# Kernel tuning notes

Measured on AMD Instinct MI355X. Metric: run time of the kernel, lower is better.

## Reference

```python
import jax, jax.numpy as jnp
import numpy as np

E = 2  # expand_ratio


def _linear_scan(u, a):
    """h_t = a_t * h_{t-1} + u_t along axis 0, h_{-1}=0. Parallel associative scan."""
    def comb(x, y):
        a1, b1 = x
        a2, b2 = y
        return a2 * a1, a2 * b1 + b2
    _, h = jax.lax.associative_scan(comb, (a, u), axis=0)
    return h


def setup_inputs() -> dict:
    key = jax.random.key(0)
    ks = jax.random.split(key, 8)
    n, b, d = 2048, 4, 1024
    s = 1.0 / np.sqrt(d)
    return {
        "x": jax.random.normal(ks[0], (n, b, d), jnp.float32),
        "lower_bound": jax.random.uniform(ks[1], (d,), jnp.float32),
        "W_in": jax.random.normal(ks[2], (d, 3 * d), jnp.float32) * s,
        "b_in": jnp.zeros((3 * d,), jnp.float32),
        "W_out": jax.random.normal(ks[3], (d, d), jnp.float32) * s,
        "b_out": jnp.zeros((d,), jnp.float32),
        "gamma": jnp.ones((d,), jnp.float32),
        "beta": jnp.zeros((d,), jnp.float32),
    }


def reference(x, lower_bound, W_in, b_in, W_out, b_out, gamma, beta):
    n, b, d = x.shape
    h = d // E
    feat = x @ W_in + b_in                      # (n,b,3d)
    inp, og, fg = jnp.split(feat, 3, axis=-1)
    inp = jax.nn.silu(inp)
    og = jax.nn.sigmoid(og)
    fg = jax.nn.sigmoid(fg)
    # reshape (h d) -> h, d=E
    inp = inp.reshape(n, b, h, E)
    og = og.reshape(n, b, h, E)
    fg = fg.reshape(n, b, h, E)
    lb = lower_bound.reshape(h, E)
    lam = lb + (1.0 - lb) * fg                  # (n,b,h,E)
    # outer-product input: (1-lam) outer inp over the E dims -> (n,b,h,E,E)
    u = jnp.einsum('nbhd,nbhe->nbhde', 1.0 - lam, inp)
    a = jnp.broadcast_to(lam[..., None], u.shape)
    u = u.reshape(n, b, h * E * E)
    a = a.reshape(n, b, h * E * E)
    state_fwd = _linear_scan(u, a)
    state_rev = jnp.flip(_linear_scan(jnp.flip(u, 0), jnp.flip(a, 0)), 0)
    state = (state_fwd + state_rev).reshape(n, b, h, E, E)
    out = jnp.einsum('nbhde,nbhd->nbhe', state, og).reshape(n, b, d)
    # layernorm over last dim
    mu = jnp.mean(out, axis=-1, keepdims=True)
    var = jnp.var(out, axis=-1, keepdims=True)
    out = (out - mu) * jax.lax.rsqrt(var + 1e-5) * gamma + beta
    return out @ W_out + b_out
```

## Files before the change

kernel.cpp:

```cpp
#include <hip/hip_runtime.h>

typedef __bf16 bf16x8 __attribute__((ext_vector_type(8)));
typedef float floatx4 __attribute__((ext_vector_type(4)));

#define NCH 128
#define CLEN 16

__device__ __forceinline__ unsigned short f2bf(float f) {
  unsigned int u = __builtin_bit_cast(unsigned int, f);
  u += 0x7fff + ((u >> 16) & 1);
  return (unsigned short)(u >> 16);
}
__device__ __forceinline__ float bf2f(unsigned short u) {
  unsigned int v = (unsigned int)u << 16;
  return __builtin_bit_cast(float, v);
}
__device__ __forceinline__ float bf2f_lo(unsigned int u) {
  return __builtin_bit_cast(float, u << 16);
}
__device__ __forceinline__ float bf2f_hi(unsigned int u) {
  return __builtin_bit_cast(float, u & 0xffff0000u);
}

__device__ __forceinline__ void async_copy16(const void* g, void* l) {
  __builtin_amdgcn_global_load_lds(
      (const __attribute__((address_space(1))) unsigned int*)g,
      (__attribute__((address_space(3))) unsigned int*)l, 16, 0, 0);
}

__global__ void cast_x_kernel(const float* __restrict__ in, unsigned short* __restrict__ out) {
  int i = blockIdx.x * blockDim.x + threadIdx.x;
  float4 v = ((const float4*)in)[i];
  ushort4 o;
  o.x = f2bf(v.x); o.y = f2bf(v.y); o.z = f2bf(v.z); o.w = f2bf(v.w);
  ((ushort4*)out)[i] = o;
}

__global__ void tcast2_kernel(const float* __restrict__ Win, unsigned short* __restrict__ winT,
                              const float* __restrict__ Wout, unsigned short* __restrict__ woutT) {
  __shared__ float tile[32][33];
  int bx = blockIdx.x;
  const float* W;
  unsigned short* WT;
  int ncols, n0;
  if (bx < 96) { W = Win; WT = winT; ncols = 3072; n0 = bx * 32; }
  else { W = Wout; WT = woutT; ncols = 1024; n0 = (bx - 96) * 32; }
  int k0 = blockIdx.y * 32;
  int tx = threadIdx.x, ty = threadIdx.y;
  tile[ty][tx] = W[(size_t)(k0 + ty) * ncols + n0 + tx];
  __syncthreads();
  WT[(size_t)(n0 + ty) * 1024 + k0 + tx] = f2bf(tile[tx][ty]);
}

template <int EPI>
__global__ __launch_bounds__(256) void gemm_kernel(
    const unsigned short* __restrict__ A, const unsigned short* __restrict__ BT,
    const float* __restrict__ bias, const float* __restrict__ lb,
    float* __restrict__ outf,
    unsigned short* __restrict__ o_inp, unsigned short* __restrict__ o_og,
    unsigned short* __restrict__ o_om) {
  __shared__ alignas(16) char smem_raw[17408];
  unsigned short* As = (unsigned short*)smem_raw;
  unsigned short* Bs = As + 128 * 32;
  const int m0 = blockIdx.x * 128, n0 = blockIdx.y * 128;
  const int tid = threadIdx.x;
  const int lane = tid & 63, wave = tid >> 6;
  const int wm = (wave >> 1) * 64, wn = (wave & 1) * 64;
  const int mrow = lane & 15, q = lane >> 4;
  const int qsw = q ^ ((mrow >> 1) & 3);
  floatx4 acc[4][4] = {};
  const int r0 = wave * 32;
  const int srow = r0 + (lane >> 2);
  const int qs = (lane & 3) ^ ((srow >> 1) & 3);
  const unsigned short* gA0 = A + (size_t)(m0 + srow) * 1024 + qs * 8;
  const unsigned short* gA1 = gA0 + (size_t)16 * 1024;
  const unsigned short* gB0 = BT + (size_t)(n0 + srow) * 1024 + qs * 8;
  const unsigned short* gB1 = gB0 + (size_t)16 * 1024;
  unsigned short* lA0 = &As[r0 * 32];
  unsigned short* lA1 = &As[(r0 + 16) * 32];
  unsigned short* lB0 = &Bs[r0 * 32];
  unsigned short* lB1 = &Bs[(r0 + 16) * 32];
  for (int kt = 0; kt < 1024; kt += 32) {
    __syncthreads();
    async_copy16(gA0, lA0);
    async_copy16(gA1, lA1);
    async_copy16(gB0, lB0);
    async_copy16(gB1, lB1);
    gA0 += 32; gA1 += 32; gB0 += 32; gB1 += 32;
    __syncthreads();
    bf16x8 af[4], bf[4];
#pragma unroll
    for (int i = 0; i < 4; i++) af[i] = *(const bf16x8*)&As[(wm + i * 16 + mrow) * 32 + qsw * 8];
#pragma unroll
    for (int j = 0; j < 4; j++) bf[j] = *(const bf16x8*)&Bs[(wn + j * 16 + mrow) * 32 + qsw * 8];
#pragma unroll
    for (int i = 0; i < 4; i++)
#pragma unroll
      for (int j = 0; j < 4; j++)
        acc[i][j] = __builtin_amdgcn_mfma_f32_16x16x32_bf16(af[i], bf[j], acc[i][j], 0, 0, 0);
  }
  const int er = tid >> 3;
  const int ec = (tid & 7) * 16;
  const int rgbase = m0 + (er & 15) + (er >> 4) * 64;
  const int lr = (wm ? 16 : 0) + q * 4;
  float bi[4];
  int cidx[4];
#pragma unroll
  for (int j = 0; j < 4; j++) {
    cidx[j] = n0 + wn + j * 16 + mrow;
    bi[j] = bias[cidx[j]];
  }
  if (EPI == 1) {
    unsigned short* Cs = (unsigned short*)smem_raw;
    const int seg = n0 >> 10;
    unsigned short* dst = (seg == 0) ? o_inp : (seg == 1) ? o_og : o_om;
    float Lv[4];
    if (seg == 2) {
#pragma unroll
      for (int j = 0; j < 4; j++) Lv[j] = lb[cidx[j] & 1023];
    }
#pragma unroll
    for (int i = 0; i < 4; i++) {
      __syncthreads();
#pragma unroll
      for (int j = 0; j < 4; j++) {
        const int lc = wn + j * 16 + mrow;
#pragma unroll
        for (int g = 0; g < 4; g++) {
          float v = acc[i][j][g] + bi[j];
          unsigned short ob;
          if (seg == 0) { float s = 1.f / (1.f + __expf(-v)); ob = f2bf(v * s); }
          else if (seg == 1) { float s = 1.f / (1.f + __expf(-v)); ob = f2bf(s); }
          else { float sm = 1.f / (1.f + __expf(v)); ob = f2bf((1.f - Lv[j]) * sm); }
          Cs[(lr + g) * 136 + lc] = ob;
        }
      }
      __syncthreads();
      uint4 v0 = *(uint4*)&Cs[er * 136 + ec];
      uint4 v1 = *(uint4*)&Cs[er * 136 + ec + 8];
      size_t ro = (size_t)(rgbase + i * 16) * 1024 + (n0 & 1023) + ec;
      *(uint4*)&dst[ro] = v0;
      *(uint4*)&dst[ro + 8] = v1;
    }
  } else {
    float* Cf = (float*)smem_raw;
#pragma unroll
    for (int i = 0; i < 4; i++) {
      __syncthreads();
#pragma unroll
      for (int j = 0; j < 4; j++) {
        const int lc = wn + j * 16 + mrow;
#pragma unroll
        for (int g = 0; g < 4; g++) Cf[(lr + g) * 132 + lc] = acc[i][j][g] + bi[j];
      }
      __syncthreads();
      size_t ro = (size_t)(rgbase + i * 16) * 1024 + n0 + ec;
#pragma unroll
      for (int k = 0; k < 4; k++) {
        float4 v = *(float4*)&Cf[er * 132 + ec + k * 4];
        *(float4*)&outf[ro + k * 4] = v;
      }
    }
  }
}

__global__ __launch_bounds__(512, 2) void gemm1_kernel(
    const unsigned short* __restrict__ A, const unsigned short* __restrict__ BT,
    const float* __restrict__ bias, const float* __restrict__ lb,
    unsigned short* __restrict__ o_inp, unsigned short* __restrict__ o_og,
    unsigned short* __restrict__ o_om) {
  __shared__ alignas(16) char smem[131072];
  const int orig = blockIdx.x;
  const int wg = (orig & 7) * 48 + (orig >> 3);
  const int m0 = (wg & 31) << 8;
  const int n0 = (wg >> 5) << 8;
  const int tid = threadIdx.x;
  const int lane = tid & 63, wave = tid >> 6;
  const int wm = wave >> 2, wn = wave & 3;
  const int srow = tid >> 3;
  const int sq = (tid & 7) ^ (srow & 7);
  const unsigned short* gA = A + (size_t)(m0 + srow) * 1024 + sq * 8;
  const unsigned short* gB = BT + (size_t)(n0 + srow) * 1024 + sq * 8;
  char* lw = smem + wave * 1024;
  const int aro = (wm * 128 + (lane & 15)) * 128;
  const int bro = (wn * 64 + (lane & 15)) * 128;
  const int qs0 = ((lane >> 4) ^ (lane & 7)) * 16;
  const int qs1 = ((4 + (lane >> 4)) ^ (lane & 7)) * 16;

  floatx4 acc[8][4] = {};
  bf16x8 aF[4][2], bF[4][2];

#define STG(lofs, gh, kk)                                \
  do {                                                   \
    const unsigned short* _g = (gh) + (size_t)(kk) * 64; \
    async_copy16(_g, lw + (lofs));                       \
    async_copy16(_g + 65536, lw + (lofs) + 8192);        \
  } while (0)
#define RA(base, mh, i, s) \
  (*(const bf16x8*)(smem + (base) + aro + (mh) * 8192 + (i) * 2048 + ((s) ? qs1 : qs0)))
#define RB(base, j, s) \
  (*(const bf16x8*)(smem + (base) + bro + (j) * 2048 + ((s) ? qs1 : qs0)))
#define BAR __builtin_amdgcn_s_barrier()
#define LGKM0 asm volatile("s_waitcnt lgkmcnt(0)" ::: "memory")
#define VM4 asm volatile("s_waitcnt vmcnt(4)" ::: "memory")
#define MM(d, a, b) d = __builtin_amdgcn_mfma_f32_16x16x32_bf16(a, b, d, 0, 0, 0)

  STG(65536, gB, 0);
  STG(65536 + 16384, gB + 131072, 0);
  STG(0, gA, 0);
  STG(0 + 16384, gA + 131072, 0);
  STG(98304, gB, 1);
  STG(98304 + 16384, gB + 131072, 1);
  VM4;
  BAR;

#pragma unroll 1
  for (int it = 0; it < 8; ++it) {
    const int t0 = 2 * it;
    const int kA1 = t0 + 1;
    const int kN2 = (t0 + 2 > 15) ? 15 : t0 + 2;
    const int kN3 = (t0 + 3 > 15) ? 15 : t0 + 3;
#pragma unroll
    for (int i = 0; i < 4; i++) { aF[i][0] = RA(0, 0, i, 0); aF[i][1] = RA(0, 0, i, 1); }
#pragma unroll
    for (int j = 0; j < 2; j++) { bF[j][0] = RB(65536, j, 0); bF[j][1] = RB(65536, j, 1); }
    STG(32768, gA, kA1);
    BAR; LGKM0;
    __builtin_amdgcn_s_setprio(1);
#pragma unroll
    for (int i = 0; i < 4; i++)
#pragma unroll
      for (int j = 0; j < 2; j++) { MM(acc[i][j], aF[i][0], bF[j][0]); MM(acc[i][j], aF[i][1], bF[j][1]); }
    __builtin_amdgcn_s_setprio(0);
    BAR;
#pragma unroll
    for (int j = 2; j < 4; j++) { bF[j][0] = RB(65536, j, 0); bF[j][1] = RB(65536, j, 1); }
    STG(32768 + 16384, gA + 131072, kA1);
    BAR; LGKM0;
    __builtin_amdgcn_s_setprio(1);
#pragma unroll
    for (int i = 0; i < 4; i++)
#pragma unroll
      for (int j = 2; j < 4; j++) { MM(acc[i][j], aF[i][0], bF[j][0]); MM(acc[i][j], aF[i][1], bF[j][1]); }
    __builtin_amdgcn_s_setprio(0);
    BAR;
#pragma unroll
    for (int i = 0; i < 4; i++) { aF[i][0] = RA(0, 1, i, 0); aF[i][1] = RA(0, 1, i, 1); }
    STG(65536, gB, kN2);
    BAR; LGKM0;
    __builtin_amdgcn_s_setprio(1);
#pragma unroll
    for (int i = 0; i < 4; i++)
#pragma unroll
      for (int j = 0; j < 2; j++) { MM(acc[4 + i][j], aF[i][0], bF[j][0]); MM(acc[4 + i][j], aF[i][1], bF[j][1]); }
    __builtin_amdgcn_s_setprio(0);
    BAR;
    STG(65536 + 16384, gB + 131072, kN2);
    BAR;
    __builtin_amdgcn_s_setprio(1);
#pragma unroll
    for (int i = 0; i < 4; i++)
#pragma unroll
      for (int j = 2; j < 4; j++) { MM(acc[4 + i][j], aF[i][0], bF[j][0]); MM(acc[4 + i][j], aF[i][1], bF[j][1]); }
    __builtin_amdgcn_s_setprio(0);
    VM4;
    BAR;
#pragma unroll
    for (int i = 0; i < 4; i++) { aF[i][0] = RA(32768, 0, i, 0); aF[i][1] = RA(32768, 0, i, 1); }
#pragma unroll
    for (int j = 0; j < 2; j++) { bF[j][0] = RB(98304, j, 0); bF[j][1] = RB(98304, j, 1); }
    STG(0, gA, kN2);
    BAR; LGKM0;
    __builtin_amdgcn_s_setprio(1);
#pragma unroll
    for (int i = 0; i < 4; i++)
#pragma unroll
      for (int j = 0; j < 2; j++) { MM(acc[i][j], aF[i][0], bF[j][0]); MM(acc[i][j], aF[i][1], bF[j][1]); }
    __builtin_amdgcn_s_setprio(0);
    BAR;
#pragma unroll
    for (int j = 2; j < 4; j++) { bF[j][0] = RB(98304, j, 0); bF[j][1] = RB(98304, j, 1); }
    STG(16384, gA + 131072, kN2);
    BAR; LGKM0;
    __builtin_amdgcn_s_setprio(1);
#pragma unroll
    for (int i = 0; i < 4; i++)
#pragma unroll
      for (int j = 2; j < 4; j++) { MM(acc[i][j], aF[i][0], bF[j][0]); MM(acc[i][j], aF[i][1], bF[j][1]); }
    __builtin_amdgcn_s_setprio(0);
    BAR;
#pragma unroll
    for (int i = 0; i < 4; i++) { aF[i][0] = RA(32768, 1, i, 0); aF[i][1] = RA(32768, 1, i, 1); }
    STG(98304, gB, kN3);
    BAR; LGKM0;
    __builtin_amdgcn_s_setprio(1);
#pragma unroll
    for (int i = 0; i < 4; i++)
#pragma unroll
      for (int j = 0; j < 2; j++) { MM(acc[4 + i][j], aF[i][0], bF[j][0]); MM(acc[4 + i][j], aF[i][1], bF[j][1]); }
    __builtin_amdgcn_s_setprio(0);
    BAR;
    STG(98304 + 16384, gB + 131072, kN3);
    BAR;
    __builtin_amdgcn_s_setprio(1);
#pragma unroll
    for (int i = 0; i < 4; i++)
#pragma unroll
      for (int j = 2; j < 4; j++) { MM(acc[4 + i][j], aF[i][0], bF[j][0]); MM(acc[4 + i][j], aF[i][1], bF[j][1]); }
    __builtin_amdgcn_s_setprio(0);
    VM4;
    BAR;
  }
#undef STG
#undef RA
#undef RB
#undef BAR
#undef LGKM0
#undef VM4
#undef MM

  asm volatile("s_waitcnt vmcnt(0) lgkmcnt(0)" ::: "memory");
  const int seg = n0 >> 10;
  unsigned short* dst = (seg == 0) ? o_inp : (seg == 1) ? o_og : o_om;
  unsigned short* Cs = (unsigned short*)smem;
  float bi[4], Lv[4];
#pragma unroll
  for (int j = 0; j < 4; j++) {
    const int c = n0 + wn * 64 + j * 16 + (lane & 15);
    bi[j] = bias[c];
    Lv[j] = (seg == 2) ? lb[c & 1023] : 0.f;
  }
  const int lrw = wm * 16 + (lane >> 4) * 4;
  const int lcw = wn * 64 + (lane & 15);
  const int er = tid >> 4, ec = (tid & 15) * 16;
  const int growb = m0 + (er >> 4) * 128 + (er & 15);
#pragma unroll
  for (int i = 0; i < 8; i++) {
    __syncthreads();
#pragma unroll
    for (int j = 0; j < 4; j++)
#pragma unroll
      for (int g = 0; g < 4; g++) {
        float v = acc[i][j][g] + bi[j];
        unsigned short ob;
        if (seg == 0) { float s = 1.f / (1.f + __expf(-v)); ob = f2bf(v * s); }
        else if (seg == 1) { float s = 1.f / (1.f + __expf(-v)); ob = f2bf(s); }
        else { float sm = 1.f / (1.f + __expf(v)); ob = f2bf((1.f - Lv[j]) * sm); }
        Cs[(lrw + g) * 264 + lcw + j * 16] = ob;
      }
    __syncthreads();
    uint4 v0 = *(uint4*)&Cs[er * 264 + ec];
    uint4 v1 = *(uint4*)&Cs[er * 264 + ec + 8];
    size_t ro = (size_t)(growb + i * 16) * 1024 + (n0 & 1023) + ec;
    *(uint4*)&dst[ro] = v0;
    *(uint4*)&dst[ro + 8] = v1;
  }
}

__global__ void scan_passA(const unsigned short* __restrict__ om, const unsigned short* __restrict__ ip,
                           float* __restrict__ sumA, float* __restrict__ sumBf,
                           float* __restrict__ sumBr) {
  int idx = blockIdx.x * 256 + threadIdx.x;
  int h = idx & 511, cb = idx >> 9, b = cb & 3, c = cb >> 2;
  long base = ((long)c * CLEN * 4 + b) * 1024 + 2 * h;
  float p0 = 1.f, p1 = 1.f;
  float s00 = 0.f, s01 = 0.f, s10 = 0.f, s11 = 0.f;
  float r00 = 0.f, r01 = 0.f, r10 = 0.f, r11 = 0.f;
#pragma unroll
  for (int t = 0; t < CLEN; t++) {
    ushort2 l2 = *(const ushort2*)(om + base);
    ushort2 i2 = *(const ushort2*)(ip + base);
    base += 4096;
    float omx = bf2f(l2.x), omy = bf2f(l2.y);
    float ipx = bf2f(i2.x), ipy = bf2f(i2.y);
    float lx = 1.f - omx, ly = 1.f - omy;
    float u00 = omx * ipx, u01 = omx * ipy, u10 = omy * ipx, u11 = omy * ipy;
    r00 += p0 * u00; r01 += p0 * u01; r10 += p1 * u10; r11 += p1 * u11;
    s00 = lx * s00 + u00; s01 = lx * s01 + u01;
    s10 = ly * s10 + u10; s11 = ly * s11 + u11;
    p0 *= lx; p1 *= ly;
  }
  ((float2*)sumA)[idx] = make_float2(p0, p1);
  ((float4*)sumBf)[idx] = make_float4(s00, s01, s10, s11);
  ((float4*)sumBr)[idx] = make_float4(r00, r01, r10, r11);
}

__global__ void scan_passB(const float* __restrict__ sumA, const float* __restrict__ sumBf,
                           const float* __restrict__ sumBr, float* __restrict__ initF,
                           float* __restrict__ initR) {
  int tid = blockIdx.x * 256 + threadIdx.x;
  int dir = tid >> 13;
  int rem = tid & 8191;
  int ch = rem & 3;
  int bh = rem >> 2;
  int dd = ch >> 1;
  if (dir == 0) {
    float H = 0.f;
    for (int c = 0; c < NCH; c++) {
      int si = c * 2048 + bh;
      initF[(size_t)si * 4 + ch] = H;
      H = sumA[(size_t)si * 2 + dd] * H + sumBf[(size_t)si * 4 + ch];
    }
  } else {
    float G = 0.f;
    for (int c = NCH - 1; c >= 0; c--) {
      int si = c * 2048 + bh;
      initR[(size_t)si * 4 + ch] = G;
      G = sumA[(size_t)si * 2 + dd] * G + sumBr[(size_t)si * 4 + ch];
    }
  }
}

__global__ __launch_bounds__(512) void scanC_ln_kernel(
    const unsigned short* __restrict__ om, const unsigned short* __restrict__ ip,
    const unsigned short* __restrict__ og,
    const float* __restrict__ initF, const float* __restrict__ initR,
    const float* __restrict__ gamma, const float* __restrict__ beta,
    unsigned short* __restrict__ ybf) {
  __shared__ float tile[8][1024];
  __shared__ float ldsG[1024];
  __shared__ float ldsB[1024];
  const int h = threadIdx.x;
  const int cb = blockIdx.x;
  const int b = cb & 3, c = cb >> 2;
  const int idx = cb * 512 + h;
  *(float2*)&ldsG[2 * h] = *(const float2*)(gamma + 2 * h);
  *(float2*)&ldsB[2 * h] = *(const float2*)(beta + 2 * h);
  float4 F = ((const float4*)initF)[idx];
  float4 R = ((const float4*)initR)[idx];
  float outx[CLEN], outy[CLEN];
  unsigned int lS[CLEN], iS[CLEN], oS[CLEN];
  const long base = ((long)c * CLEN * 4 + b) * 1024 + 2 * h;
  float h00 = F.x, h01 = F.y, h10 = F.z, h11 = F.w;
  long p = base;
#pragma unroll
  for (int t = 0; t < CLEN; t++) {
    unsigned int l2 = *(const unsigned int*)(om + p);
    unsigned int i2 = *(const unsigned int*)(ip + p);
    unsigned int o2 = *(const unsigned int*)(og + p);
    p += 4096;
    lS[t] = l2; iS[t] = i2; oS[t] = o2;
    float omx = bf2f_lo(l2), omy = bf2f_hi(l2);
    float ipx = bf2f_lo(i2), ipy = bf2f_hi(i2);
    float ox = bf2f_lo(o2), oy = bf2f_hi(o2);
    float lx = 1.f - omx, ly = 1.f - omy;
    h00 = lx * h00 + omx * ipx; h01 = lx * h01 + omx * ipy;
    h10 = ly * h10 + omy * ipx; h11 = ly * h11 + omy * ipy;
    outx[t] = h00 * ox + h10 * oy;
    outy[t] = h01 * ox + h11 * oy;
  }
  float g00 = R.x, g01 = R.y, g10 = R.z, g11 = R.w;
#pragma unroll
  for (int t = CLEN - 1; t >= 0; t--) {
    unsigned int l2 = lS[t], i2 = iS[t], o2 = oS[t];
    float omx = bf2f_lo(l2), omy = bf2f_hi(l2);
    float ipx = bf2f_lo(i2), ipy = bf2f_hi(i2);
    float ox = bf2f_lo(o2), oy = bf2f_hi(o2);
    float lx = 1.f - omx, ly = 1.f - omy;
    g00 = omx * ipx + lx * g00; g01 = omx * ipy + lx * g01;
    g10 = omy * ipx + ly * g10; g11 = omy * ipy + ly * g11;
    outx[t] += g00 * ox + g10 * oy;
    outy[t] += g01 * ox + g11 * oy;
  }
  const int lane = h & 63, wv = h >> 6;
#pragma unroll
  for (int g = 0; g < CLEN / 8; g++) {
    __syncthreads();
#pragma unroll
    for (int r = 0; r < 8; r++) {
      float2 v2 = make_float2(outx[g * 8 + r], outy[g * 8 + r]);
      *(float2*)&tile[r][2 * h] = v2;
    }
    __syncthreads();
    {
      const int t = g * 8 + wv;
      float4 v[4];
#pragma unroll
      for (int k = 0; k < 4; k++) v[k] = *(const float4*)&tile[wv][lane * 16 + k * 4];
      float s = 0.f, s2 = 0.f;
#pragma unroll
      for (int k = 0; k < 4; k++) {
        s += v[k].x + v[k].y + v[k].z + v[k].w;
        s2 += v[k].x * v[k].x + v[k].y * v[k].y + v[k].z * v[k].z + v[k].w * v[k].w;
      }
#pragma unroll
      for (int off = 1; off < 64; off <<= 1) {
        s += __shfl_xor(s, off);
        s2 += __shfl_xor(s2, off);
      }
      float mean = s * (1.f / 1024.f);
      float var = s2 * (1.f / 1024.f) - mean * mean;
      float rstd = rsqrtf(var + 1e-5f);
      unsigned short o16[16];
#pragma unroll
      for (int k = 0; k < 4; k++) {
        float* vv = (float*)&v[k];
#pragma unroll
        for (int e = 0; e < 4; e++) {
          int ch = lane * 16 + k * 4 + e;
          o16[k * 4 + e] = f2bf((vv[e] - mean) * rstd * ldsG[ch] + ldsB[ch]);
        }
      }
      size_t rowo = ((size_t)(c * CLEN + t) * 4 + b) * 1024 + lane * 16;
      *(uint4*)(ybf + rowo) = *(uint4*)&o16[0];
      *(uint4*)(ybf + rowo + 8) = *(uint4*)&o16[8];
    }
  }
}

extern "C" void kernel_launch(void* const* d_in, const int* in_sizes, int n_in,
                              void* d_out, int out_size, void* d_ws, size_t ws_size,
                              hipStream_t stream) {
  const float* x = (const float*)d_in[0];
  const float* lb = (const float*)d_in[1];
  const float* Win = (const float*)d_in[2];
  const float* bin = (const float*)d_in[3];
  const float* Wout = (const float*)d_in[4];
  const float* bout = (const float*)d_in[5];
  const float* gamma = (const float*)d_in[6];
  const float* beta = (const float*)d_in[7];
  float* out = (float*)d_out;

  char* ws = (char*)d_ws;
  size_t off = 0;
  auto alloc = [&](size_t bytes) {
    void* p = ws + off;
    off += (bytes + 255) & ~(size_t)255;
    return p;
  };
  unsigned short* x_bf = (unsigned short*)alloc(8192ull * 1024 * 2);
  unsigned short* winT = (unsigned short*)alloc(3072ull * 1024 * 2);
  unsigned short* woutT = (unsigned short*)alloc(1024ull * 1024 * 2);
  unsigned short* inp_b = (unsigned short*)alloc(8192ull * 1024 * 2);
  unsigned short* og_b = (unsigned short*)alloc(8192ull * 1024 * 2);
  unsigned short* om_b = (unsigned short*)alloc(8192ull * 1024 * 2);
  unsigned short* y_bf = (unsigned short*)alloc(8192ull * 1024 * 2);
  float* sumA = (float*)alloc((size_t)NCH * 4 * 512 * 2 * 4);
  float* sumBf = (float*)alloc((size_t)NCH * 4 * 512 * 4 * 4);
  float* sumBr = (float*)alloc((size_t)NCH * 4 * 512 * 4 * 4);
  float* initF = (float*)alloc((size_t)NCH * 4 * 512 * 4 * 4);
  float* initR = (float*)alloc((size_t)NCH * 4 * 512 * 4 * 4);

  cast_x_kernel<<<8192, 256, 0, stream>>>(x, x_bf);
  tcast2_kernel<<<dim3(128, 32), dim3(32, 32), 0, stream>>>(Win, winT, Wout, woutT);
  gemm1_kernel<<<384, 512, 0, stream>>>(x_bf, winT, bin, lb, inp_b, og_b, om_b);
  scan_passA<<<(NCH * 4 * 512) / 256, 256, 0, stream>>>(om_b, inp_b, sumA, sumBf, sumBr);
  scan_passB<<<64, 256, 0, stream>>>(sumA, sumBf, sumBr, initF, initR);
  scanC_ln_kernel<<<NCH * 4, 512, 0, stream>>>(om_b, inp_b, og_b, initF, initR, gamma, beta, y_bf);
  gemm_kernel<0><<<dim3(64, 8), 256, 0, stream>>>(y_bf, woutT, bout, nullptr, out, nullptr, nullptr, nullptr);
}
```

Before: 258.6 us.

## Split serial chunk-prefix scan into three-level hierarchical scan

The single scan_passB kernel, which walked all 128 chunk summaries serially with only 16K threads in 64 blocks, is replaced by three kernels. They compute 8 super-chunk summaries of 16 chunks each, scan those 8 serially, then rescan each super-chunk to write the per-chunk initial states. Serial depth drops from 128 to 16+8+16 steps and the busy grids grow to 512 blocks, improving GPU occupancy. In exchange it adds two kernel launches and extra global traffic for the intermediate buffers.

```diff
diff --git a/kernel.cpp b/kernel.cpp
--- a/kernel.cpp
+++ b/kernel.cpp
@@ -385,28 +385,72 @@
   ((float4*)sumBr)[idx] = make_float4(r00, r01, r10, r11);
 }
 
-__global__ void scan_passB(const float* __restrict__ sumA, const float* __restrict__ sumBf,
-                           const float* __restrict__ sumBr, float* __restrict__ initF,
-                           float* __restrict__ initR) {
-  int tid = blockIdx.x * 256 + threadIdx.x;
-  int dir = tid >> 13;
-  int rem = tid & 8191;
-  int ch = rem & 3;
-  int bh = rem >> 2;
+__global__ void scan_b1(const float* __restrict__ sumA, const float* __restrict__ sumBf,
+                        const float* __restrict__ sumBr,
+                        float* __restrict__ superA, float* __restrict__ superB) {
+  int t = blockIdx.x * 256 + threadIdx.x;
+  int ch = t & 3, bh = (t >> 2) & 2047, sc = (t >> 13) & 7, dir = t >> 16;
   int dd = ch >> 1;
+  float Acc = 1.f, Bcc = 0.f;
   if (dir == 0) {
-    float H = 0.f;
-    for (int c = 0; c < NCH; c++) {
-      int si = c * 2048 + bh;
+    for (int i = 0; i < 16; i++) {
+      int si = (sc * 16 + i) * 2048 + bh;
+      float a = sumA[(size_t)si * 2 + dd];
+      float b = sumBf[(size_t)si * 4 + ch];
+      Bcc = a * Bcc + b;
+      Acc *= a;
+    }
+  } else {
+    for (int i = 15; i >= 0; i--) {
+      int si = (sc * 16 + i) * 2048 + bh;
+      float a = sumA[(size_t)si * 2 + dd];
+      float b = sumBr[(size_t)si * 4 + ch];
+      Bcc = a * Bcc + b;
+      Acc *= a;
+    }
+  }
+  superA[t] = Acc;
+  superB[t] = Bcc;
+}
+
+__global__ void scan_b2(const float* __restrict__ superA, const float* __restrict__ superB,
+                        float* __restrict__ SI) {
+  int t = blockIdx.x * 256 + threadIdx.x;
+  int ch = t & 3, bh = (t >> 2) & 2047, dir = t >> 13;
+  float H = 0.f;
+  if (dir == 0) {
+    for (int sc = 0; sc < 8; sc++) {
+      size_t idx = ((size_t)(dir * 8 + sc) * 2048 + bh) * 4 + ch;
+      SI[idx] = H;
+      H = superA[idx] * H + superB[idx];
+    }
+  } else {
+    for (int sc = 7; sc >= 0; sc--) {
+      size_t idx = ((size_t)(dir * 8 + sc) * 2048 + bh) * 4 + ch;
+      SI[idx] = H;
+      H = superA[idx] * H + superB[idx];
+    }
+  }
+}
+
+__global__ void scan_b3(const float* __restrict__ sumA, const float* __restrict__ sumBf,
+                        const float* __restrict__ sumBr, const float* __restrict__ SI,
+                        float* __restrict__ initF, float* __restrict__ initR) {
+  int t = blockIdx.x * 256 + threadIdx.x;
+  int ch = t & 3, bh = (t >> 2) & 2047, sc = (t >> 13) & 7, dir = t >> 16;
+  int dd = ch >> 1;
+  float H = SI[t];
+  if (dir == 0) {
+    for (int i = 0; i < 16; i++) {
+      int si = (sc * 16 + i) * 2048 + bh;
       initF[(size_t)si * 4 + ch] = H;
       H = sumA[(size_t)si * 2 + dd] * H + sumBf[(size_t)si * 4 + ch];
     }
   } else {
-    float G = 0.f;
-    for (int c = NCH - 1; c >= 0; c--) {
-      int si = c * 2048 + bh;
-      initR[(size_t)si * 4 + ch] = G;
-      G = sumA[(size_t)si * 2 + dd] * G + sumBr[(size_t)si * 4 + ch];
+    for (int i = 15; i >= 0; i--) {
+      int si = (sc * 16 + i) * 2048 + bh;
+      initR[(size_t)si * 4 + ch] = H;
+      H = sumA[(size_t)si * 2 + dd] * H + sumBr[(size_t)si * 4 + ch];
     }
   }
 }
@@ -540,12 +584,17 @@
   float* sumBr = (float*)alloc((size_t)NCH * 4 * 512 * 4 * 4);
   float* initF = (float*)alloc((size_t)NCH * 4 * 512 * 4 * 4);
   float* initR = (float*)alloc((size_t)NCH * 4 * 512 * 4 * 4);
+  float* superA = (float*)alloc(131072ull * 4);
+  float* superB = (float*)alloc(131072ull * 4);
+  float* SIbuf = (float*)alloc(131072ull * 4);
 
   cast_x_kernel<<<8192, 256, 0, stream>>>(x, x_bf);
   tcast2_kernel<<<dim3(128, 32), dim3(32, 32), 0, stream>>>(Win, winT, Wout, woutT);
   gemm1_kernel<<<384, 512, 0, stream>>>(x_bf, winT, bin, lb, inp_b, og_b, om_b);
   scan_passA<<<(NCH * 4 * 512) / 256, 256, 0, stream>>>(om_b, inp_b, sumA, sumBf, sumBr);
-  scan_passB<<<64, 256, 0, stream>>>(sumA, sumBf, sumBr, initF, initR);
+  scan_b1<<<512, 256, 0, stream>>>(sumA, sumBf, sumBr, superA, superB);
+  scan_b2<<<64, 256, 0, stream>>>(superA, superB, SIbuf);
+  scan_b3<<<512, 256, 0, stream>>>(sumA, sumBf, sumBr, SIbuf, initF, initR);
   scanC_ln_kernel<<<NCH * 4, 512, 0, stream>>>(om_b, inp_b, og_b, initF, initR, gamma, beta, y_bf);
   gemm_kernel<0><<<dim3(64, 8), 256, 0, stream>>>(y_bf, woutT, bout, nullptr, out, nullptr, nullptr, nullptr);
 }
```

After: 261.8 us. Within noise of the previous version (+1.2%).
